# Performance work log

Hardware: AMD Instinct MI355X
Metric: run time of the kernel (lower is better)

Reference implementation:

```python
import jax, jax.numpy as jnp
import numpy as np
import math

C = 512
EPS = 1e-5


def _ln(x, g, b):
    m = jnp.mean(x, axis=-1, keepdims=True)
    v = jnp.var(x, axis=-1, keepdims=True)
    return (x - m) * jax.lax.rsqrt(v + EPS) * g + b


def _attn(x, w_qkv, w_out):
    # x: (..., L, C); attention over axis -2 (axial)
    qkv = jnp.einsum('...lc,dc->...ld', x, w_qkv)          # (..., L, 3C)
    qkv = qkv.reshape(*qkv.shape[:-1], C, 3)               # interleaved split as in torch reshape(*shape,3)
    q, k, v = qkv[..., 0], qkv[..., 1], qkv[..., 2]
    scale = 1.0 / math.sqrt(C)
    logits = jnp.einsum('...qc,...kc->...qk', q, k) * scale
    p = jax.nn.softmax(logits, axis=-1)
    ctx = jnp.einsum('...qk,...kc->...qc', p, v)
    return jnp.einsum('...lc,dc->...ld', ctx, w_out)


def setup_inputs() -> dict:
    key = jax.random.key(0)
    ks = jax.random.split(key, 16)
    s = 0.02
    inp = {
        'x': jax.random.normal(ks[0], (8, C, 48, 192), jnp.float32),
        'w_qkv1': jax.random.normal(ks[1], (3 * C, C), jnp.float32) * s,
        'w_out1': jax.random.normal(ks[2], (C, C), jnp.float32) * s,
        'w_qkv2': jax.random.normal(ks[3], (3 * C, C), jnp.float32) * s,
        'w_out2': jax.random.normal(ks[4], (C, C), jnp.float32) * s,
        'g1': jnp.ones((C,), jnp.float32), 'b1': jnp.zeros((C,), jnp.float32),
        'g2': jnp.ones((C,), jnp.float32), 'b2': jnp.zeros((C,), jnp.float32),
        'g3': jnp.ones((C,), jnp.float32), 'b3': jnp.zeros((C,), jnp.float32),
        'w_fc1': jax.random.normal(ks[5], (4 * C, C), jnp.float32) * s,
        'b_fc1': jnp.zeros((4 * C,), jnp.float32),
        'w_fc2': jax.random.normal(ks[6], (C, 4 * C), jnp.float32) * s,
        'b_fc2': jnp.zeros((C,), jnp.float32),
    }
    return inp


def reference(x, w_qkv1, w_out1, w_qkv2, w_out2, g1, b1, g2, b2, g3, b3,
              w_fc1, b_fc1, w_fc2, b_fc2):
    # x: (B, C, H, W) -> (B, W, H, C)
    x = jnp.transpose(x, (0, 3, 2, 1))
    x = x + _attn(_ln(x, g1, b1), w_qkv1, w_out1)          # attention along H
    # (B, W, H, C) -> (B, H, W, C)
    x = jnp.transpose(x, (0, 2, 1, 3))
    x = x + _attn(_ln(x, g2, b2), w_qkv2, w_out2)          # attention along W
    h = _ln(x, g3, b3)
    h = jax.nn.relu(jnp.einsum('bhwc,dc->bhwd', h, w_fc1) + b_fc1)
    x = x + jnp.einsum('bhwd,cd->bhwc', h, w_fc2) + b_fc2
    # (B, H, W, C) -> (B, C, H, W)
    return jnp.transpose(x, (0, 3, 1, 2))
```

## Files before the change

kernel.cpp:

```cpp
#include <hip/hip_runtime.h>

typedef unsigned short u16;
typedef __attribute__((ext_vector_type(8))) short short8;
typedef __attribute__((ext_vector_type(8))) __bf16 bf16x8;
typedef __attribute__((ext_vector_type(4))) float f32x4;

#define DEV __device__ __forceinline__

DEV u16 f2bf(float f){ unsigned u = __float_as_uint(f); return (u16)((u + 0x7fffu + ((u>>16)&1u)) >> 16); }
DEV float bf2f(u16 h){ return __uint_as_float(((unsigned)h)<<16); }

DEV f32x4 mfma_bf16(short8 a, short8 b, f32x4 c){
  return __builtin_amdgcn_mfma_f32_16x16x32_bf16(
      __builtin_bit_cast(bf16x8, a), __builtin_bit_cast(bf16x8, b), c, 0, 0, 0);
}

DEV void gl2lds16(const u16* g, u16* s){
  __builtin_amdgcn_global_load_lds(
      (__attribute__((address_space(1))) void*)(g),
      (__attribute__((address_space(3))) void*)(s), 16, 0, 0);
}

#define BB 8
#define HH 48
#define WW 192
#define CC 512
#define NTOK (BB*HH*WW)

__global__ void k_permqkv(const float* __restrict__ w, u16* __restrict__ o){
  int i = blockIdx.x*256 + threadIdx.x;
  int n = i >> 9, kk = i & 511;
  int src = 3*(n & 511) + (n >> 9);
  o[i] = f2bf(w[src*512 + kk]);
}
__global__ void k_conv(const float* __restrict__ w, u16* __restrict__ o, int nelem){
  int i = blockIdx.x*256 + threadIdx.x;
  if (i < nelem) o[i] = f2bf(w[i]);
}

__global__ void k_tin(const float* __restrict__ x, float* __restrict__ xr){
  __shared__ float T[32][33];
  int bh = blockIdx.x / 96, rem = blockIdx.x % 96;
  int c0 = (rem/6)*32, w0 = (rem%6)*32;
  int b = bh / HH, h = bh % HH;
  const float* xp = x + ((size_t)b*CC*HH + h)*WW;
  #pragma unroll
  for (int p=0;p<4;p++){
    int idx = p*256 + threadIdx.x;
    int cc = idx >> 5, ww = idx & 31;
    T[cc][ww] = xp[(size_t)(c0+cc)*(HH*WW) + w0 + ww];
  }
  __syncthreads();
  float* xo = xr + (size_t)bh*WW*CC;
  #pragma unroll
  for (int p=0;p<4;p++){
    int idx = p*256 + threadIdx.x;
    int ww = idx >> 5, cc = idx & 31;
    xo[(size_t)(w0+ww)*CC + c0 + cc] = T[cc][ww];
  }
}

__global__ void k_tout(const float* __restrict__ xr, float* __restrict__ out){
  __shared__ float T[32][33];
  int bh = blockIdx.x / 96, rem = blockIdx.x % 96;
  int c0 = (rem/6)*32, w0 = (rem%6)*32;
  int b = bh / HH, h = bh % HH;
  const float* xi = xr + (size_t)bh*WW*CC;
  #pragma unroll
  for (int p=0;p<4;p++){
    int idx = p*256 + threadIdx.x;
    int ww = idx >> 5, cc = idx & 31;
    T[ww][cc] = xi[(size_t)(w0+ww)*CC + c0 + cc];
  }
  __syncthreads();
  float* op = out + ((size_t)b*CC*HH + h)*WW;
  #pragma unroll
  for (int p=0;p<4;p++){
    int idx = p*256 + threadIdx.x;
    int cc = idx >> 5, ww = idx & 31;
    op[(size_t)(c0+cc)*(HH*WW) + w0 + ww] = T[ww][cc];
  }
}

__global__ void k_ln(const float* __restrict__ xr, const float* __restrict__ g,
                     const float* __restrict__ bb, u16* __restrict__ y){
  int t = blockIdx.x*4 + (threadIdx.x>>6);
  int lane = threadIdx.x & 63;
  const float* row = xr + (size_t)t*CC + lane*8;
  float v[8];
  *(f32x4*)(v)   = *(const f32x4*)(row);
  *(f32x4*)(v+4) = *(const f32x4*)(row+4);
  float s=0.f, s2=0.f;
  #pragma unroll
  for (int j=0;j<8;j++){ s += v[j]; s2 += v[j]*v[j]; }
  #pragma unroll
  for (int o=32;o;o>>=1){ s += __shfl_xor(s,o); s2 += __shfl_xor(s2,o); }
  float mean = s*(1.f/CC);
  float var  = s2*(1.f/CC) - mean*mean;
  float rs = rsqrtf(var + 1e-5f);
  const float* gp = g + lane*8; const float* bp = bb + lane*8;
  short8 o8;
  #pragma unroll
  for (int j=0;j<8;j++) o8[j] = (short)f2bf((v[j]-mean)*rs*gp[j] + bp[j]);
  *(short8*)(y + (size_t)t*CC + lane*8) = o8;
}

__global__ __launch_bounds__(256)
void k_gemm(const u16* __restrict__ A, int lda,
            const u16* __restrict__ Bw, int ldb,
            void* __restrict__ Out, int ldo,
            const float* __restrict__ bias,
            int K, int nbn, int epi){
  __shared__ __align__(16) u16 As[128*64];
  __shared__ __align__(16) u16 Bs[128*64];
  int cpx = gridDim.x >> 3;
  int l = (blockIdx.x & 7)*cpx + (blockIdx.x >> 3);
  int mb = l / nbn, nb = l % nbn;
  int tid = threadIdx.x, lane = tid & 63, wv = tid >> 6;
  size_t m0 = (size_t)mb*128, n0 = (size_t)nb*128;
  int lr = lane >> 3;
  int cc0 = (lane & 7) ^ lr;
  const u16* gA = A  + (m0 + wv*32 + lr)*(size_t)lda + cc0*8;
  const u16* gB = Bw + (n0 + wv*32 + lr)*(size_t)ldb + cc0*8;
  u16* sA = As + wv*32*64;
  u16* sB = Bs + wv*32*64;
  int m = lane & 15, quad = lane >> 4;
  int wm = (wv>>1)*64, wn = (wv&1)*64;
  int off0 = ((quad    ) ^ (m & 7))*8;
  int off1 = ((quad + 4) ^ (m & 7))*8;
  f32x4 acc[4][4];
  #pragma unroll
  for (int i=0;i<4;i++)
    #pragma unroll
    for (int j=0;j<4;j++) acc[i][j] = (f32x4){0.f,0.f,0.f,0.f};
  const u16* aB = As + (wm + m)*64;
  const u16* bB = Bs + (wn + m)*64;
  for (int k0 = 0; k0 < K; k0 += 64){
    #pragma unroll
    for (int t=0;t<4;t++){
      gl2lds16(gA + (size_t)(t*8)*lda, sA + t*8*64);
      gl2lds16(gB + (size_t)(t*8)*ldb, sB + t*8*64);
    }
    gA += 64; gB += 64;
    __syncthreads();
    {
      short8 af[4], bf[4];
      #pragma unroll
      for (int i=0;i<4;i++) af[i] = *(const short8*)(aB + i*16*64 + off0);
      #pragma unroll
      for (int j=0;j<4;j++) bf[j] = *(const short8*)(bB + j*16*64 + off0);
      #pragma unroll
      for (int i=0;i<4;i++)
        #pragma unroll
        for (int j=0;j<4;j++)
          acc[i][j] = mfma_bf16(af[i], bf[j], acc[i][j]);
    }
    {
      short8 af[4], bf[4];
      #pragma unroll
      for (int i=0;i<4;i++) af[i] = *(const short8*)(aB + i*16*64 + off1);
      #pragma unroll
      for (int j=0;j<4;j++) bf[j] = *(const short8*)(bB + j*16*64 + off1);
      #pragma unroll
      for (int i=0;i<4;i++)
        #pragma unroll
        for (int j=0;j<4;j++)
          acc[i][j] = mfma_bf16(af[i], bf[j], acc[i][j]);
    }
    __syncthreads();
  }
  if (epi == 2){
    float* O = (float*)Out + (m0 + wm + quad*4)*(size_t)ldo + n0 + wn + m;
    #pragma unroll
    for (int j=0;j<4;j++){
      float bv = bias ? bias[n0 + wn + j*16 + m] : 0.f;
      #pragma unroll
      for (int i=0;i<4;i++)
        #pragma unroll
        for (int r=0;r<4;r++)
          O[(size_t)(i*16+r)*ldo + j*16] += acc[i][j][r] + bv;
    }
  } else {
    u16* O = (u16*)Out + (m0 + wm + quad*4)*(size_t)ldo + n0 + wn + m;
    #pragma unroll
    for (int j=0;j<4;j++){
      float bv = bias ? bias[n0 + wn + j*16 + m] : 0.f;
      #pragma unroll
      for (int i=0;i<4;i++)
        #pragma unroll
        for (int r=0;r<4;r++){
          float v = acc[i][j][r] + bv;
          if (epi == 1) v = fmaxf(v, 0.f);
          O[(size_t)(i*16+r)*ldo + j*16] = f2bf(v);
        }
    }
  }
}

template<int L, int RPB, int KCH, int NW>
__global__ __launch_bounds__(64*NW)
void k_qk2(const u16* __restrict__ q, const u16* __restrict__ kp, int ldq,
           float* __restrict__ S, int SD, int OUTs, int INN, int LST, float scale){
  constexpr int NSTRIP = L / RPB;
  constexpr int NCH = L / KCH;
  constexpr int RPW = KCH / NW;
  constexpr int NJT = KCH / 16;
  __shared__ __align__(16) u16 Ks[KCH*512];
  int cpx = gridDim.x >> 3;
  int bl = (blockIdx.x & 7)*cpx + (blockIdx.x >> 3);
  int s = bl / NSTRIP, st = bl % NSTRIP;
  int lane = threadIdx.x & 63, wv = threadIdx.x >> 6;
  int m = lane & 15, quad = lane >> 4;
  size_t tokbase = (size_t)(s/SD)*OUTs + (size_t)(s%SD)*INN;

  const u16* qr = q + (tokbase + (size_t)(st*RPB + wv*16 + m)*LST)*ldq + quad*8;
  short8 qf[16];
  #pragma unroll
  for (int kk=0;kk<16;kk++) qf[kk] = *(const short8*)(qr + kk*32);

  float* Sp = S + (size_t)s*L*L + (size_t)(st*RPB + wv*16 + quad*4)*L;

  for (int ch = 0; ch < NCH; ch++){
    #pragma unroll
    for (int rr = 0; rr < RPW; rr++){
      int row = wv*RPW + rr;
      gl2lds16(kp + (tokbase + (size_t)(ch*KCH + row)*LST)*ldq + (lane ^ (row & 7))*8,
               Ks + row*512);
    }
    asm volatile("s_waitcnt vmcnt(0)" ::: "memory");
    __syncthreads();

    f32x4 acc[NJT];
    #pragma unroll
    for (int jt=0;jt<NJT;jt++) acc[jt] = (f32x4){0.f,0.f,0.f,0.f};
    const u16* kB = Ks + m*512;
    #pragma unroll
    for (int kk=0;kk<16;kk++){
      int chunk = ((quad + kk*4) ^ (m & 7))*8;
      #pragma unroll
      for (int jt=0;jt<NJT;jt++){
        short8 bf = *(const short8*)(kB + jt*16*512 + chunk);
        acc[jt] = mfma_bf16(qf[kk], bf, acc[jt]);
      }
    }
    #pragma unroll
    for (int jt=0;jt<NJT;jt++)
      #pragma unroll
      for (int r=0;r<4;r++)
        Sp[(size_t)r*L + ch*KCH + jt*16 + m] = acc[jt][r]*scale;
    if (ch + 1 < NCH) __syncthreads();
  }
}

__global__ void k_softmax(const float* __restrict__ S, u16* __restrict__ P, int L, int Lp){
  int row = blockIdx.x*4 + (threadIdx.x>>6);
  int lane = threadIdx.x & 63;
  const float* sr = S + (size_t)row*L;
  float v0 = (lane      < L) ? sr[lane]      : -3.0e38f;
  float v1 = (lane+64   < L) ? sr[lane+64]   : -3.0e38f;
  float v2 = (lane+128  < L) ? sr[lane+128]  : -3.0e38f;
  float mx = fmaxf(v0, fmaxf(v1, v2));
  #pragma unroll
  for (int o=32;o;o>>=1) mx = fmaxf(mx, __shfl_xor(mx, o));
  float e0 = (lane      < L) ? __expf(v0-mx) : 0.f;
  float e1 = (lane+64   < L) ? __expf(v1-mx) : 0.f;
  float e2 = (lane+128  < L) ? __expf(v2-mx) : 0.f;
  float sm = e0+e1+e2;
  #pragma unroll
  for (int o=32;o;o>>=1) sm += __shfl_xor(sm, o);
  float inv = 1.f/sm;
  u16* pr = P + (size_t)row*Lp;
  if (lane      < Lp) pr[lane]      = f2bf(e0*inv);
  if (lane+64   < Lp) pr[lane+64]   = f2bf(e1*inv);
  if (lane+128  < Lp) pr[lane+128]  = f2bf(e2*inv);
}

__global__ void k_vt(const u16* __restrict__ v, int ldv, u16* __restrict__ vt,
                     int L, int Lp, int SD, int OUTs, int INN, int LST){
  __shared__ float T[32*193];
  int s = blockIdx.x >> 4;
  int c0 = (blockIdx.x & 15)*32;
  size_t tokbase = (size_t)(s/SD)*OUTs + (size_t)(s%SD)*INN;
  int pad = Lp + 1;
  for (int idx = threadIdx.x; idx < L*32; idx += 256){
    int l = idx >> 5, cc = idx & 31;
    T[cc*pad + l] = bf2f(v[(tokbase + (size_t)l*LST)*ldv + c0 + cc]);
  }
  __syncthreads();
  u16* vo = vt + ((size_t)s*CC + c0)*Lp;
  for (int idx = threadIdx.x; idx < 32*Lp; idx += 256){
    int cc = idx / Lp, l = idx - cc*Lp;
    vo[idx] = (l < L) ? f2bf(T[cc*pad + l]) : (u16)0;
  }
}

template<int L, int Lp, int NTQ, int NCJ>
__global__ __launch_bounds__(256)
void k_pv2(const u16* __restrict__ P, const u16* __restrict__ vt, u16* __restrict__ ctx,
           int SD, int OUTs, int INN, int LST){
  constexpr int G   = 32 / NCJ;
  constexpr int LPP = Lp + 8;
  constexpr int CW  = NCJ * 16;
  constexpr int CJW = NCJ / 4;
  constexpr int NKS = Lp / 32;
  constexpr int SHW = (L*LPP > L*CW) ? L*LPP : L*CW;
  __shared__ __align__(16) u16 SH[SHW];

  int sq = blockIdx.x / G, g = blockIdx.x % G;
  int tid = threadIdx.x, lane = tid & 63, wv = tid >> 6;
  int m = lane & 15, quad = lane >> 4;

  const u16* Pg = P + (size_t)sq * L * Lp;
  constexpr int PU = L * Lp / 8;
  for (int u = tid; u < PU; u += 256){
    int r = u / (Lp/8), c = u % (Lp/8);
    *(short8*)(SH + r*LPP + c*8) = *(const short8*)(Pg + (size_t)r*Lp + c*8);
  }
  __syncthreads();

  short8 bfr[CJW][NKS];
  #pragma unroll
  for (int lc = 0; lc < CJW; lc++){
    const u16* vr = vt + ((size_t)sq*CC + (size_t)((g*NCJ + (wv*CJW + lc))*16 + m))*Lp + quad*8;
    #pragma unroll
    for (int ks = 0; ks < NKS; ks++) bfr[lc][ks] = *(const short8*)(vr + ks*32);
  }

  f32x4 acc[CJW][NTQ];
  #pragma unroll
  for (int lc = 0; lc < CJW; lc++)
    #pragma unroll
    for (int qt = 0; qt < NTQ; qt++) acc[lc][qt] = (f32x4){0.f,0.f,0.f,0.f};

  #pragma unroll
  for (int qt = 0; qt < NTQ; qt++){
    short8 a[NKS];
    #pragma unroll
    for (int ks = 0; ks < NKS; ks++)
      a[ks] = *(const short8*)(SH + (qt*16 + m)*LPP + quad*8 + ks*32);
    #pragma unroll
    for (int lc = 0; lc < CJW; lc++)
      #pragma unroll
      for (int ks = 0; ks < NKS; ks++)
        acc[lc][qt] = mfma_bf16(a[ks], bfr[lc][ks], acc[lc][qt]);
  }
  __syncthreads();

  #pragma unroll
  for (int qt = 0; qt < NTQ; qt++)
    #pragma unroll
    for (int lc = 0; lc < CJW; lc++)
      #pragma unroll
      for (int r = 0; r < 4; r++)
        SH[(qt*16 + quad*4 + r)*CW + (wv*CJW + lc)*16 + m] = f2bf(acc[lc][qt][r]);
  __syncthreads();

  size_t tokbase = (size_t)(sq/SD)*OUTs + (size_t)(sq%SD)*INN;
  constexpr int CU8 = CW / 8;
  constexpr int TU = L * CU8;
  for (int u = tid; u < TU; u += 256){
    int l = u / CU8, c = u % CU8;
    *(short8*)(ctx + (tokbase + (size_t)l*LST)*CC + g*CW + c*8) =
        *(const short8*)(SH + l*CW + c*8);
  }
}

extern "C" void kernel_launch(void* const* d_in, const int* in_sizes, int n_in,
                              void* d_out, int out_size, void* d_ws, size_t ws_size,
                              hipStream_t stream){
  const float* x      = (const float*)d_in[0];
  const float* wqkv1  = (const float*)d_in[1];
  const float* wout1  = (const float*)d_in[2];
  const float* wqkv2  = (const float*)d_in[3];
  const float* wout2  = (const float*)d_in[4];
  const float* g1 = (const float*)d_in[5];  const float* b1 = (const float*)d_in[6];
  const float* g2 = (const float*)d_in[7];  const float* b2 = (const float*)d_in[8];
  const float* g3 = (const float*)d_in[9];  const float* b3 = (const float*)d_in[10];
  const float* wfc1 = (const float*)d_in[11]; const float* bfc1 = (const float*)d_in[12];
  const float* wfc2 = (const float*)d_in[13]; const float* bfc2 = (const float*)d_in[14];

  char* ws = (char*)d_ws;
  size_t off = 0;
  auto alloc = [&](size_t bytes)->char*{
    char* p = ws + off; off += (bytes + 255) & ~(size_t)255; return p;
  };
  float* xres = (float*)alloc((size_t)NTOK*CC*4);
  u16*   y    = (u16*)  alloc((size_t)NTOK*CC*2);
  u16*   qkv  = (u16*)  alloc((size_t)NTOK*1536*2);
  u16* wqkv1p = (u16*)alloc((size_t)1536*512*2);
  u16* wqkv2p = (u16*)alloc((size_t)1536*512*2);
  u16* wout1p = (u16*)alloc((size_t)512*512*2);
  u16* wout2p = (u16*)alloc((size_t)512*512*2);
  u16* wfc1p  = (u16*)alloc((size_t)2048*512*2);
  u16* wfc2p  = (u16*)alloc((size_t)512*2048*2);
  u16*   hv   = qkv;

  u16*   P    = (u16*)d_out;
  u16*   vt   = (u16*)((char*)d_out + 28311552);
  float* S    = (float*)((char*)d_out + 28311552);
  (void)ws_size; (void)in_sizes; (void)n_in; (void)out_size;

  const float scale = 0.044194173824159216f;

  k_permqkv<<<3072, 256, 0, stream>>>(wqkv1, wqkv1p);
  k_permqkv<<<3072, 256, 0, stream>>>(wqkv2, wqkv2p);
  k_conv<<<1024, 256, 0, stream>>>(wout1, wout1p, 512*512);
  k_conv<<<1024, 256, 0, stream>>>(wout2, wout2p, 512*512);
  k_conv<<<4096, 256, 0, stream>>>(wfc1, wfc1p, 2048*512);
  k_conv<<<4096, 256, 0, stream>>>(wfc2, wfc2p, 512*2048);

  k_tin<<<BB*HH*96, 256, 0, stream>>>(x, xres);

  k_ln<<<NTOK/4, 256, 0, stream>>>(xres, g1, b1, y);
  k_gemm<<<576*12, 256, 0, stream>>>(y, 512, wqkv1p, 512, qkv, 1536, nullptr, 512, 12, 0);
  k_qk2<48,48,48,3><<<1536, 192, 0, stream>>>(qkv, qkv+512, 1536, S, 192, 9216, 1, 192, scale);
  k_softmax<<<NTOK/4, 256, 0, stream>>>(S, P, 48, 64);
  k_vt<<<1536*16, 256, 0, stream>>>(qkv+1024, 1536, vt, 48, 64, 192, 9216, 1, 192);
  k_pv2<48,64,3,16><<<1536*2, 256, 0, stream>>>(P, vt, y, 192, 9216, 1, 192);
  k_gemm<<<576*4, 256, 0, stream>>>(y, 512, wout1p, 512, xres, 512, nullptr, 512, 4, 2);

  k_ln<<<NTOK/4, 256, 0, stream>>>(xres, g2, b2, y);
  k_gemm<<<576*12, 256, 0, stream>>>(y, 512, wqkv2p, 512, qkv, 1536, nullptr, 512, 12, 0);
  k_qk2<192,64,64,4><<<1152, 256, 0, stream>>>(qkv, qkv+512, 1536, S, 48, 9216, 192, 1, scale);
  k_softmax<<<NTOK/4, 256, 0, stream>>>(S, P, 192, 192);
  k_vt<<<384*16, 256, 0, stream>>>(qkv+1024, 1536, vt, 192, 192, 48, 9216, 192, 1);
  k_pv2<192,192,12,8><<<384*4, 256, 0, stream>>>(P, vt, y, 48, 9216, 192, 1);
  k_gemm<<<576*4, 256, 0, stream>>>(y, 512, wout2p, 512, xres, 512, nullptr, 512, 4, 2);

  k_ln<<<NTOK/4, 256, 0, stream>>>(xres, g3, b3, y);
  for (int half = 0; half < 2; half++){
    size_t M0 = (size_t)half * 36864;
    k_gemm<<<288*16, 256, 0, stream>>>(y + M0*512, 512, wfc1p, 512, hv, 2048, bfc1, 512, 16, 1);
    k_gemm<<<288*4, 256, 0, stream>>>(hv, 2048, wfc2p, 2048, xres + M0*512, 512, bfc2, 2048, 4, 2);
  }

  k_tout<<<BB*HH*96, 256, 0, stream>>>(xres, (float*)d_out);
}
```

Baseline: 2.009 ms.

## Add 256x256-tile double-buffered bf16 GEMM with phased MFMA/LDS scheduling for large projections

Introduces a new 512-thread GEMM kernel with 256x256 output tiles, double-buffered LDS staging through direct global-to-LDS loads, and an XOR-swizzled layout. The K loop is split into four quadrant phases with explicit barriers, wait counts and setprio so MFMA work overlaps the prefetch of the tile two steps ahead. The QKV projections and both MLP GEMMs now use it, cutting per-FLOP global and LDS traffic compared with the smaller-tile kernel. The costs are 128 KB of LDS per block and fewer blocks per launch (as few as 288 for fc2), which may reduce occupancy and leave a partial last wave.

```diff
diff --git a/kernel.cpp b/kernel.cpp
--- a/kernel.cpp
+++ b/kernel.cpp
@@ -197,6 +197,169 @@
   }
 }
 
+template<int EPI>
+__global__ __launch_bounds__(512, 2)
+void k_gemm256(const u16* __restrict__ A, int lda,
+               const u16* __restrict__ Bw, int ldb,
+               void* __restrict__ Out, int ldo,
+               const float* __restrict__ bias,
+               int K, int nbn){
+  __shared__ __align__(16) u16 As[2*16384];
+  __shared__ __align__(16) u16 Bs[2*16384];
+  const int tid = threadIdx.x, lane = tid & 63, wv = tid >> 6;
+  const int m = lane & 15, quad = lane >> 4;
+  const int wr = wv >> 2, wc = wv & 3;
+  const int cpx = gridDim.x >> 3;
+  const int bl = (blockIdx.x & 7)*cpx + (blockIdx.x >> 3);
+  const int mb = bl / nbn, nb = bl % nbn;
+  const size_t m0 = (size_t)mb * 256, n0 = (size_t)nb * 256;
+
+  const int srow = wv*8 + (lane >> 3);
+  const int schk = ((lane & 7) ^ (lane >> 3)) * 8;
+  const u16* gA = A  + (m0 + srow) * (size_t)lda + schk;
+  const u16* gB = Bw + (n0 + srow) * (size_t)ldb + schk;
+  const int sdst = wv * 8 * 64;
+  const int NT = K >> 6;
+
+#define STG_A(bufi, tt, p) gl2lds16(gA + (size_t)(p)*64*lda + (size_t)(tt)*64, \
+                                    As + (bufi)*16384 + (p)*4096 + sdst)
+#define STG_B(bufi, tt, p) gl2lds16(gB + (size_t)(p)*64*ldb + (size_t)(tt)*64, \
+                                    Bs + (bufi)*16384 + (p)*4096 + sdst)
+#define WAIT_LGKM0 asm volatile("s_waitcnt lgkmcnt(0)" ::: "memory")
+#define WAIT_VM8   asm volatile("s_waitcnt vmcnt(8)" ::: "memory")
+#define WAIT_VM0   asm volatile("s_waitcnt vmcnt(0)" ::: "memory")
+#define SCHED0 __builtin_amdgcn_sched_barrier(0)
+#define BAR    __builtin_amdgcn_s_barrier()
+#define PRIO1  __builtin_amdgcn_s_setprio(1)
+#define PRIO0  __builtin_amdgcn_s_setprio(0)
+
+  STG_A(0,0,0); STG_A(0,0,1); STG_A(0,0,2); STG_A(0,0,3);
+  STG_B(0,0,0); STG_B(0,0,1); STG_B(0,0,2); STG_B(0,0,3);
+  STG_B(1,1,0); STG_B(1,1,1); STG_B(1,1,2); STG_B(1,1,3);
+  STG_A(1,1,0); STG_A(1,1,1); STG_A(1,1,2); STG_A(1,1,3);
+
+  f32x4 acc[8][4];
+  #pragma unroll
+  for (int i=0;i<8;i++)
+    #pragma unroll
+    for (int j=0;j<4;j++) acc[i][j] = (f32x4){0.f,0.f,0.f,0.f};
+
+  const int off0 = ( quad      ^ (m & 7)) * 8;
+  const int off1 = ((quad + 4) ^ (m & 7)) * 8;
+
+  WAIT_VM8;
+  BAR;
+
+  for (int t = 0; t < NT; ++t){
+    const int buf = t & 1;
+    const u16* aB = As + buf*16384 + (wr*128 + m)*64;
+    const u16* bB = Bs + buf*16384 + (wc*64  + m)*64;
+    short8 avlo[4][2], avhi[4][2], bvlo[2][2], bvhi[2][2];
+
+    #pragma unroll
+    for (int i=0;i<4;i++){
+      avlo[i][0] = *(const short8*)(aB + i*1024 + off0);
+      avlo[i][1] = *(const short8*)(aB + i*1024 + off1);
+    }
+    #pragma unroll
+    for (int j=0;j<2;j++){
+      bvlo[j][0] = *(const short8*)(bB + j*1024 + off0);
+      bvlo[j][1] = *(const short8*)(bB + j*1024 + off1);
+    }
+    BAR; WAIT_LGKM0; SCHED0;
+    PRIO1;
+    #pragma unroll
+    for (int i=0;i<4;i++)
+      #pragma unroll
+      for (int j=0;j<2;j++){
+        acc[i][j] = mfma_bf16(avlo[i][0], bvlo[j][0], acc[i][j]);
+        acc[i][j] = mfma_bf16(avlo[i][1], bvlo[j][1], acc[i][j]);
+      }
+    PRIO0;
+    BAR;
+
+    #pragma unroll
+    for (int j=0;j<2;j++){
+      bvhi[j][0] = *(const short8*)(bB + (2+j)*1024 + off0);
+      bvhi[j][1] = *(const short8*)(bB + (2+j)*1024 + off1);
+    }
+    BAR; WAIT_LGKM0; SCHED0;
+    PRIO1;
+    #pragma unroll
+    for (int i=0;i<4;i++)
+      #pragma unroll
+      for (int j=0;j<2;j++){
+        acc[i][2+j] = mfma_bf16(avlo[i][0], bvhi[j][0], acc[i][2+j]);
+        acc[i][2+j] = mfma_bf16(avlo[i][1], bvhi[j][1], acc[i][2+j]);
+      }
+    PRIO0;
+    BAR;
+
+    #pragma unroll
+    for (int i=0;i<4;i++){
+      avhi[i][0] = *(const short8*)(aB + (4+i)*1024 + off0);
+      avhi[i][1] = *(const short8*)(aB + (4+i)*1024 + off1);
+    }
+    if (t + 2 < NT){ STG_B(buf,t+2,0); STG_B(buf,t+2,1); STG_B(buf,t+2,2); STG_B(buf,t+2,3); }
+    BAR; WAIT_LGKM0; SCHED0;
+    PRIO1;
+    #pragma unroll
+    for (int i=0;i<4;i++)
+      #pragma unroll
+      for (int j=0;j<2;j++){
+        acc[4+i][2+j] = mfma_bf16(avhi[i][0], bvhi[j][0], acc[4+i][2+j]);
+        acc[4+i][2+j] = mfma_bf16(avhi[i][1], bvhi[j][1], acc[4+i][2+j]);
+      }
+    PRIO0;
+    BAR;
+
+    if (t + 2 < NT){ STG_A(buf,t+2,0); STG_A(buf,t+2,1); STG_A(buf,t+2,2); STG_A(buf,t+2,3); }
+    BAR;
+    PRIO1;
+    #pragma unroll
+    for (int i=0;i<4;i++)
+      #pragma unroll
+      for (int j=0;j<2;j++){
+        acc[4+i][j] = mfma_bf16(avhi[i][0], bvlo[j][0], acc[4+i][j]);
+        acc[4+i][j] = mfma_bf16(avhi[i][1], bvlo[j][1], acc[4+i][j]);
+      }
+    PRIO0;
+    if (t + 2 < NT)      { WAIT_VM8; SCHED0; }
+    else if (t + 1 < NT) { WAIT_VM0; SCHED0; }
+    if (t + 1 < NT) BAR;
+  }
+
+#undef STG_A
+#undef STG_B
+
+  if (EPI == 2){
+    float* O = (float*)Out + (m0 + wr*128 + quad*4)*(size_t)ldo + n0 + wc*64 + m;
+    #pragma unroll
+    for (int j=0;j<4;j++){
+      float bvv = bias ? bias[n0 + wc*64 + j*16 + m] : 0.f;
+      #pragma unroll
+      for (int i=0;i<8;i++)
+        #pragma unroll
+        for (int r=0;r<4;r++)
+          O[(size_t)(i*16+r)*ldo + j*16] += acc[i][j][r] + bvv;
+    }
+  } else {
+    u16* O = (u16*)Out + (m0 + wr*128 + quad*4)*(size_t)ldo + n0 + wc*64 + m;
+    #pragma unroll
+    for (int j=0;j<4;j++){
+      float bvv = bias ? bias[n0 + wc*64 + j*16 + m] : 0.f;
+      #pragma unroll
+      for (int i=0;i<8;i++)
+        #pragma unroll
+        for (int r=0;r<4;r++){
+          float v = acc[i][j][r] + bvv;
+          if (EPI == 1) v = fmaxf(v, 0.f);
+          O[(size_t)(i*16+r)*ldo + j*16] = f2bf(v);
+        }
+    }
+  }
+}
+
 template<int L, int RPB, int KCH, int NW>
 __global__ __launch_bounds__(64*NW)
 void k_qk2(const u16* __restrict__ q, const u16* __restrict__ kp, int ldq,
@@ -412,7 +575,7 @@
   k_tin<<<BB*HH*96, 256, 0, stream>>>(x, xres);
 
   k_ln<<<NTOK/4, 256, 0, stream>>>(xres, g1, b1, y);
-  k_gemm<<<576*12, 256, 0, stream>>>(y, 512, wqkv1p, 512, qkv, 1536, nullptr, 512, 12, 0);
+  k_gemm256<0><<<288*6, 512, 0, stream>>>(y, 512, wqkv1p, 512, qkv, 1536, nullptr, 512, 6);
   k_qk2<48,48,48,3><<<1536, 192, 0, stream>>>(qkv, qkv+512, 1536, S, 192, 9216, 1, 192, scale);
   k_softmax<<<NTOK/4, 256, 0, stream>>>(S, P, 48, 64);
   k_vt<<<1536*16, 256, 0, stream>>>(qkv+1024, 1536, vt, 48, 64, 192, 9216, 1, 192);
@@ -420,7 +583,7 @@
   k_gemm<<<576*4, 256, 0, stream>>>(y, 512, wout1p, 512, xres, 512, nullptr, 512, 4, 2);
 
   k_ln<<<NTOK/4, 256, 0, stream>>>(xres, g2, b2, y);
-  k_gemm<<<576*12, 256, 0, stream>>>(y, 512, wqkv2p, 512, qkv, 1536, nullptr, 512, 12, 0);
+  k_gemm256<0><<<288*6, 512, 0, stream>>>(y, 512, wqkv2p, 512, qkv, 1536, nullptr, 512, 6);
   k_qk2<192,64,64,4><<<1152, 256, 0, stream>>>(qkv, qkv+512, 1536, S, 48, 9216, 192, 1, scale);
   k_softmax<<<NTOK/4, 256, 0, stream>>>(S, P, 192, 192);
   k_vt<<<384*16, 256, 0, stream>>>(qkv+1024, 1536, vt, 192, 192, 48, 9216, 192, 1);
@@ -430,8 +593,8 @@
   k_ln<<<NTOK/4, 256, 0, stream>>>(xres, g3, b3, y);
   for (int half = 0; half < 2; half++){
     size_t M0 = (size_t)half * 36864;
-    k_gemm<<<288*16, 256, 0, stream>>>(y + M0*512, 512, wfc1p, 512, hv, 2048, bfc1, 512, 16, 1);
-    k_gemm<<<288*4, 256, 0, stream>>>(hv, 2048, wfc2p, 2048, xres + M0*512, 512, bfc2, 2048, 4, 2);
+    k_gemm256<1><<<144*8, 512, 0, stream>>>(y + M0*512, 512, wfc1p, 512, hv, 2048, bfc1, 512, 8);
+    k_gemm256<2><<<144*2, 512, 0, stream>>>(hv, 2048, wfc2p, 2048, xres + M0*512, 512, bfc2, 2048, 2);
   }
 
   k_tout<<<BB*HH*96, 256, 0, stream>>>(xres, (float*)d_out);
```

After: 2.157 ms. +7.4%, slower.
